# Kernel optimization log

Hardware: AMD Instinct MI355X
Metric: run time of the kernel (lower is better)

The kernel has to match this reference:

```python
import jax, jax.numpy as jnp
import numpy as np

C = 256
GROUPS = 8
EPS = 1e-5

def group_norm(x, gamma, beta):
    # x: [B, C, L]
    B, Cc, L = x.shape
    xg = x.reshape(B, GROUPS, Cc // GROUPS, L)
    mu = xg.mean(axis=(2, 3), keepdims=True)
    var = xg.var(axis=(2, 3), keepdims=True)
    xn = (xg - mu) / jnp.sqrt(var + EPS)
    xn = xn.reshape(B, Cc, L)
    return xn * gamma[None, :, None] + beta[None, :, None]

def conv1x1(x, W, b):
    # W: [Cout, Cin], x: [B, Cin, L]
    return jnp.einsum('oc,bcl->bol', W, x) + b[None, :, None]

def setup_inputs() -> dict:
    key = jax.random.key(0)
    ks = jax.random.split(key, 11)
    s = 1.0 / np.sqrt(C)
    inp = {
        'x': jax.random.normal(ks[0], (8, C, 2048), dtype=jnp.float32),
        'gamma': jnp.ones((C,), jnp.float32),
        'beta': jnp.zeros((C,), jnp.float32),
        'Wq': jax.random.uniform(ks[1], (C, C), jnp.float32, -s, s),
        'bq': jax.random.uniform(ks[2], (C,), jnp.float32, -s, s),
        'Wk': jax.random.uniform(ks[3], (C, C), jnp.float32, -s, s),
        'bk': jax.random.uniform(ks[4], (C,), jnp.float32, -s, s),
        'Wv': jax.random.uniform(ks[5], (C, C), jnp.float32, -s, s),
        'bv': jax.random.uniform(ks[6], (C,), jnp.float32, -s, s),
        'Wo': jax.random.uniform(ks[7], (C, C), jnp.float32, -s, s),
        'bo': jax.random.uniform(ks[8], (C,), jnp.float32, -s, s),
    }
    return inp

def reference(x, gamma, beta, Wq, bq, Wk, bk, Wv, bv, Wo, bo):
    h = group_norm(x, gamma, beta)
    q = conv1x1(h, Wq, bq)  # [B, C, L]
    k = conv1x1(h, Wk, bk)
    v = conv1x1(h, Wv, bv)
    scale = x.shape[1] ** (-0.5)
    attn = jnp.einsum('bci,bcj->bij', q, k) * scale  # [B, L, L]
    attn = jax.nn.softmax(attn, axis=-1)
    out = jnp.einsum('bij,bcj->bci', attn, v)  # [B, C, L]
    out = conv1x1(out, Wo, bo)
    return x + out
```

## Files before the change

### kernel.cpp

```cpp
#include <hip/hip_runtime.h>
#include <hip/hip_bf16.h>
#include <stddef.h>

#define NB 8
#define NC 256
#define NL 2048

typedef __attribute__((ext_vector_type(8))) short s16x8;
typedef __attribute__((ext_vector_type(4))) float f32x4;

__device__ __forceinline__ short f2bs(float x){
  __hip_bfloat16 h = __float2bfloat16(x);
  return __builtin_bit_cast(short, h);
}
__device__ __forceinline__ float bs2f(short x){
  unsigned u = ((unsigned)(unsigned short)x) << 16;
  return __builtin_bit_cast(float, u);
}

#define MFMA16(a,b,c) __builtin_amdgcn_mfma_f32_16x16x32_bf16((a),(b),(c),0,0,0)

__global__ void k_prep(const float* __restrict__ wq, const float* __restrict__ wk,
                       const float* __restrict__ wv, const float* __restrict__ wo,
                       short* __restrict__ wout){
  int idx = blockIdx.x * 256 + threadIdx.x;
  int which = idx >> 16;
  int off = idx & 65535;
  const float* src = (which == 0) ? wq : (which == 1) ? wk : (which == 2) ? wv : wo;
  float sc = (which == 0) ? 0.0625f : 1.0f;
  wout[idx] = f2bs(src[off] * sc);
}

__global__ __launch_bounds__(256) void k_stats(const float* __restrict__ x, float* __restrict__ gpart){
  const int idx = blockIdx.x;
  const float4* base = (const float4*)(x + (size_t)idx * 8192);
  const int t = threadIdx.x;
  float s = 0.f, ss = 0.f;
  for (int i = t; i < 2048; i += 256){
    float4 v = base[i];
    s  += v.x + v.y + v.z + v.w;
    ss += v.x*v.x + v.y*v.y + v.z*v.z + v.w*v.w;
  }
  #pragma unroll
  for (int m = 32; m; m >>= 1){ s += __shfl_down(s, m); ss += __shfl_down(ss, m); }
  __shared__ float red[8];
  if ((t & 63) == 0){ red[t >> 6] = s; red[4 + (t >> 6)] = ss; }
  __syncthreads();
  if (t == 0){
    gpart[idx * 2 + 0] = red[0] + red[1] + red[2] + red[3];
    gpart[idx * 2 + 1] = red[4] + red[5] + red[6] + red[7];
  }
}

__global__ __launch_bounds__(256) void k_gapply(const float* __restrict__ x, const float* __restrict__ gamma,
                                                const float* __restrict__ beta, const float* __restrict__ gpart,
                                                short* __restrict__ ht){
  const int idx = blockIdx.x;
  const int bg = idx >> 3, lt8 = idx & 7;
  const int b = bg >> 3, g = bg & 7;
  float S = 0.f, SS = 0.f;
  #pragma unroll
  for (int s2 = 0; s2 < 8; ++s2){ S += gpart[(bg * 8 + s2) * 2]; SS += gpart[(bg * 8 + s2) * 2 + 1]; }
  const float mu = S * (1.f / 65536.f);
  const float var = SS * (1.f / 65536.f) - mu * mu;
  const float rstd = rsqrtf(var + 1e-5f);
  const float* xg = x + (size_t)bg * 65536;
  const int t = threadIdx.x;
  const int cc = t >> 3, lch = t & 7;
  const int c = g * 32 + cc;
  const float gsc = gamma[c] * rstd;
  const float gbi = beta[c] - mu * gsc;
  __shared__ short tile[64 * 33];
  const int ll_s = t & 63, cg = t >> 6;
  for (int lt = 0; lt < 4; ++lt){
    const int l0 = lt8 * 256 + lt * 64;
    const float4* rp = (const float4*)(xg + (size_t)cc * NL + l0 + lch * 8);
    float4 a = rp[0], bv = rp[1];
    float vals[8] = {a.x, a.y, a.z, a.w, bv.x, bv.y, bv.z, bv.w};
    short o[8];
    #pragma unroll
    for (int e = 0; e < 8; ++e) o[e] = f2bs(vals[e] * gsc + gbi);
    __syncthreads();
    #pragma unroll
    for (int e = 0; e < 8; ++e) tile[(lch * 8 + e) * 33 + cc] = o[e];
    __syncthreads();
    s16x8 pk;
    #pragma unroll
    for (int e = 0; e < 8; ++e) pk[e] = tile[ll_s * 33 + cg * 8 + e];
    *(s16x8*)(ht + ((size_t)(b * NL) + l0 + ll_s) * NC + g * 32 + cg * 8) = pk;
  }
}

__global__ __launch_bounds__(256) void k_conv_qk(const short* __restrict__ ht, const short* __restrict__ wbf,
                                                 const float* __restrict__ bq, const float* __restrict__ bk,
                                                 short* __restrict__ qt, short* __restrict__ kt){
  const int b = blockIdx.z & 7, which = blockIdx.z >> 3;
  const short* wmat = wbf + (which ? 65536 : 0);
  const float* bias = which ? bk : bq;
  const float bsc = which ? 1.0f : 0.0625f;
  short* outp = which ? kt : qt;
  const int lane = threadIdx.x & 63, wid = threadIdx.x >> 6;
  const int wr = wid >> 1, wc = wid & 1;
  const int l0 = blockIdx.y * 128 + wr * 64;
  const int o0 = blockIdx.x * 64 + wc * 32;
  const int kgrp = (lane >> 4) * 8;
  const short* aptr = ht + ((size_t)(b * NL) + l0 + (lane & 15)) * NC + kgrp;
  const short* bptr = wmat + (size_t)(o0 + (lane & 15)) * NC + kgrp;
  f32x4 acc[4][2];
  #pragma unroll
  for (int i = 0; i < 4; ++i){
    #pragma unroll
    for (int j = 0; j < 2; ++j){ f32x4 z = {0.f,0.f,0.f,0.f}; acc[i][j] = z; }
  }
  #pragma unroll 2
  for (int kk = 0; kk < 256; kk += 32){
    s16x8 af[4], bfr[2];
    #pragma unroll
    for (int mf = 0; mf < 4; ++mf) af[mf] = *(const s16x8*)(aptr + (size_t)(mf * 16) * NC + kk);
    #pragma unroll
    for (int nf = 0; nf < 2; ++nf) bfr[nf] = *(const s16x8*)(bptr + (size_t)(nf * 16) * NC + kk);
    #pragma unroll
    for (int mf = 0; mf < 4; ++mf)
      #pragma unroll
      for (int nf = 0; nf < 2; ++nf)
        acc[mf][nf] = MFMA16(af[mf], bfr[nf], acc[mf][nf]);
  }
  #pragma unroll
  for (int nf = 0; nf < 2; ++nf){
    const int oc = o0 + nf * 16 + (lane & 15);
    const float bb = bias[oc] * bsc;
    #pragma unroll
    for (int mf = 0; mf < 4; ++mf){
      #pragma unroll
      for (int r = 0; r < 4; ++r){
        const int lr = l0 + mf * 16 + (lane >> 4) * 4 + r;
        outp[((size_t)(b * NL) + lr) * NC + oc] = f2bs(acc[mf][nf][r] + bb);
      }
    }
  }
}

__global__ __launch_bounds__(256) void k_conv_v(const short* __restrict__ ht, const short* __restrict__ wv,
                                                const float* __restrict__ bv, short* __restrict__ vout){
  const int b = blockIdx.z;
  const int lane = threadIdx.x & 63, wid = threadIdx.x >> 6;
  const int wr = wid >> 1, wc = wid & 1;
  const int o0 = blockIdx.y * 128 + wr * 64;
  const int l0 = blockIdx.x * 64 + wc * 32;
  const int kgrp = (lane >> 4) * 8;
  const short* aptr = wv + (size_t)(o0 + (lane & 15)) * NC + kgrp;
  const short* bptr = ht + ((size_t)(b * NL) + l0 + (lane & 15)) * NC + kgrp;
  f32x4 acc[4][2];
  #pragma unroll
  for (int i = 0; i < 4; ++i){
    #pragma unroll
    for (int j = 0; j < 2; ++j){ f32x4 z = {0.f,0.f,0.f,0.f}; acc[i][j] = z; }
  }
  #pragma unroll 2
  for (int kk = 0; kk < 256; kk += 32){
    s16x8 af[4], bfr[2];
    #pragma unroll
    for (int mf = 0; mf < 4; ++mf) af[mf] = *(const s16x8*)(aptr + (size_t)(mf * 16) * NC + kk);
    #pragma unroll
    for (int nf = 0; nf < 2; ++nf) bfr[nf] = *(const s16x8*)(bptr + (size_t)(nf * 16) * NC + kk);
    #pragma unroll
    for (int mf = 0; mf < 4; ++mf)
      #pragma unroll
      for (int nf = 0; nf < 2; ++nf)
        acc[mf][nf] = MFMA16(af[mf], bfr[nf], acc[mf][nf]);
  }
  #pragma unroll
  for (int mf = 0; mf < 4; ++mf){
    #pragma unroll
    for (int r = 0; r < 4; ++r){
      const int orow = o0 + mf * 16 + (lane >> 4) * 4 + r;
      const float bb = bv[orow];
      #pragma unroll
      for (int nf = 0; nf < 2; ++nf){
        const int lcol = l0 + nf * 16 + (lane & 15);
        vout[((size_t)(b * NC) + orow) * NL + lcol] = f2bs(acc[mf][nf][r] + bb);
      }
    }
  }
}

__global__ __launch_bounds__(256, 2) void k_flash(const short* __restrict__ qt, const short* __restrict__ kt,
                                                  const short* __restrict__ v, short* __restrict__ po,
                                                  float* __restrict__ ml){
  const int flat = blockIdx.x;
  const int b = flat & 7;
  const int rest = flat >> 3;
  const int h = rest & 1;
  const int i0 = (rest >> 1) * 64;
  const int lane = threadIdx.x & 63, wid = threadIdx.x >> 6;
  __shared__ short k_lds[64 * 256];
  __shared__ short v_lds[256 * 64];
  __shared__ short plds[4][1024];
  short* pl = plds[wid];
  const int arow = lane & 15, kg = lane >> 4;

  const short* qp = qt + ((size_t)(b * NL) + i0 + wid * 16 + arow) * NC + kg * 8;
  s16x8 qf[8];
  #pragma unroll
  for (int kc = 0; kc < 8; ++kc) qf[kc] = *(const s16x8*)(qp + kc * 32);

  f32x4 oacc[16];
  #pragma unroll
  for (int i = 0; i < 16; ++i){ f32x4 z = {0.f,0.f,0.f,0.f}; oacc[i] = z; }
  float m_r[4], l_r[4];
  #pragma unroll
  for (int r = 0; r < 4; ++r){ m_r[r] = -3.0e38f; l_r[r] = 0.f; }

  auto STAGE_K = [&](int jt){
    const int j0 = jt * 64;
    #pragma unroll
    for (int t = 0; t < 8; ++t){
      const int i = wid * 8 + t;
      const int r = 2 * i + (lane >> 5);
      const int wb = (lane & 31) * 16;
      const short* src = kt + ((size_t)(b * NL) + j0 + r) * NC + ((wb ^ ((r & 15) << 4)) >> 1);
      __builtin_amdgcn_global_load_lds((const __attribute__((address_space(1))) void*)src,
                                       (__attribute__((address_space(3))) void*)&k_lds[i * 512], 16, 0, 0);
    }
  };
  auto STAGE_V = [&](int jt){
    const int j0 = jt * 64;
    #pragma unroll
    for (int t = 0; t < 8; ++t){
      const int i = wid * 8 + t;
      const int rc = 8 * i + (lane >> 3);
      const int wb = (lane & 7) * 16;
      const short* src = v + ((size_t)(b * NC) + rc) * NL + j0 + ((wb ^ ((rc & 7) << 4)) >> 1);
      __builtin_amdgcn_global_load_lds((const __attribute__((address_space(1))) void*)src,
                                       (__attribute__((address_space(3))) void*)&v_lds[i * 512], 16, 0, 0);
    }
  };

  const int jb0 = h * 16, jend = jb0 + 16;
  STAGE_K(jb0);
  STAGE_V(jb0);
  asm volatile("s_waitcnt vmcnt(0)" ::: "memory");
  __builtin_amdgcn_s_barrier();
  __builtin_amdgcn_sched_barrier(0);

  for (int jt = jb0; jt < jend; ++jt){
    f32x4 sf[4];
    #pragma unroll
    for (int nf = 0; nf < 4; ++nf){ f32x4 z = {0.f,0.f,0.f,0.f}; sf[nf] = z; }
    __builtin_amdgcn_s_setprio(1);
    #pragma unroll
    for (int kc = 0; kc < 8; ++kc){
      #pragma unroll
      for (int nf = 0; nf < 4; ++nf){
        const int r = nf * 16 + arow;
        s16x8 kf = *(const s16x8*)&k_lds[r * 256 + (((kc * 64 + kg * 16) ^ ((arow & 15) << 4)) >> 1)];
        sf[nf] = MFMA16(qf[kc], kf, sf[nf]);
      }
    }
    __builtin_amdgcn_s_setprio(0);
    float corr[4];
    #pragma unroll
    for (int r = 0; r < 4; ++r){
      float mx = fmaxf(fmaxf(sf[0][r], sf[1][r]), fmaxf(sf[2][r], sf[3][r]));
      #pragma unroll
      for (int d = 1; d < 16; d <<= 1) mx = fmaxf(mx, __shfl_xor(mx, d));
      const float mn = fmaxf(m_r[r], mx);
      corr[r] = __expf(m_r[r] - mn);
      float rs = 0.f;
      #pragma unroll
      for (int nf = 0; nf < 4; ++nf){
        float p = __expf(sf[nf][r] - mn);
        sf[nf][r] = p;
        rs += p;
      }
      #pragma unroll
      for (int d = 1; d < 16; d <<= 1) rs += __shfl_xor(rs, d);
      l_r[r] = l_r[r] * corr[r] + rs;
      m_r[r] = mn;
    }
    #pragma unroll
    for (int i = 0; i < 16; ++i){
      f32x4 t = oacc[i];
      t[0] *= corr[0]; t[1] *= corr[1]; t[2] *= corr[2]; t[3] *= corr[3];
      oacc[i] = t;
    }
    asm volatile("s_waitcnt vmcnt(0)" ::: "memory");
    __builtin_amdgcn_s_barrier();
    __builtin_amdgcn_sched_barrier(0);
    if (jt + 1 < jend) STAGE_K(jt + 1);

    #pragma unroll
    for (int r = 0; r < 4; ++r){
      const int rowp = kg * 4 + r;
      const int swz = (rowp & 7) << 3;
      #pragma unroll
      for (int nf = 0; nf < 4; ++nf){
        const int col = nf * 16 + arow;
        pl[rowp * 64 + (col ^ swz)] = f2bs(sf[nf][r]);
      }
    }
    __builtin_amdgcn_s_setprio(1);
    #pragma unroll
    for (int kc2 = 0; kc2 < 2; ++kc2){
      const int swz2 = (arow & 7) << 3;
      s16x8 pa = *(const s16x8*)(pl + arow * 64 + ((kc2 * 32 + kg * 8) ^ swz2));
      #pragma unroll
      for (int nf2 = 0; nf2 < 16; ++nf2){
        const int rc = nf2 * 16 + arow;
        s16x8 vf = *(const s16x8*)&v_lds[rc * 64 + (((kc2 * 64 + kg * 16) ^ ((rc & 7) << 4)) >> 1)];
        oacc[nf2] = MFMA16(pa, vf, oacc[nf2]);
      }
    }
    __builtin_amdgcn_s_setprio(0);
    __builtin_amdgcn_s_barrier();
    __builtin_amdgcn_sched_barrier(0);
    if (jt + 1 < jend) STAGE_V(jt + 1);
    asm volatile("s_waitcnt vmcnt(8)" ::: "memory");
    __builtin_amdgcn_s_barrier();
    __builtin_amdgcn_sched_barrier(0);
  }

  short* pob = po + (size_t)h * 4194304 + ((size_t)(b * NL) + i0 + wid * 16) * NC;
  #pragma unroll
  for (int r = 0; r < 4; ++r){
    const int irow = kg * 4 + r;
    #pragma unroll
    for (int nf2 = 0; nf2 < 16; ++nf2){
      pob[(size_t)irow * NC + nf2 * 16 + arow] = f2bs(oacc[nf2][r]);
    }
    if (arow == 0){
      const size_t Rg = (size_t)h * 16384 + (size_t)(b * NL) + i0 + wid * 16 + irow;
      ml[Rg * 2 + 0] = m_r[r];
      ml[Rg * 2 + 1] = l_r[r];
    }
  }
}

__global__ __launch_bounds__(256) void k_final(const short* __restrict__ po, const float* __restrict__ ml,
                                               const short* __restrict__ wo, const float* __restrict__ bo,
                                               const float* __restrict__ x, float* __restrict__ out){
  const int b = blockIdx.z;
  const int lane = threadIdx.x & 63, wid = threadIdx.x >> 6;
  const int wr = wid >> 1, wc = wid & 1;
  const int o0 = blockIdx.y * 128 + wr * 64;
  const int i0 = blockIdx.x * 64 + wc * 32;
  const int kgrp = (lane >> 4) * 8;
  const short* aptr = wo + (size_t)(o0 + (lane & 15)) * NC + kgrp;
  float wgt[2][2], winv[2];
  size_t rbase[2];
  #pragma unroll
  for (int nf = 0; nf < 2; ++nf){
    const int Rg = b * NL + i0 + nf * 16 + (lane & 15);
    rbase[nf] = (size_t)Rg * NC + kgrp;
    const float m0 = ml[(size_t)Rg * 2],             l0 = ml[(size_t)Rg * 2 + 1];
    const float m1 = ml[((size_t)16384 + Rg) * 2],   l1 = ml[((size_t)16384 + Rg) * 2 + 1];
    const float mm = fmaxf(m0, m1);
    wgt[nf][0] = __expf(m0 - mm);
    wgt[nf][1] = __expf(m1 - mm);
    winv[nf] = 1.f / (l0 * wgt[nf][0] + l1 * wgt[nf][1]);
  }
  f32x4 acc[4][2];
  #pragma unroll
  for (int i = 0; i < 4; ++i){
    #pragma unroll
    for (int j = 0; j < 2; ++j){ f32x4 z = {0.f,0.f,0.f,0.f}; acc[i][j] = z; }
  }
  for (int kk = 0; kk < 256; kk += 32){
    s16x8 af[4], bfr[2];
    #pragma unroll
    for (int mf = 0; mf < 4; ++mf) af[mf] = *(const s16x8*)(aptr + (size_t)(mf * 16) * NC + kk);
    #pragma unroll
    for (int nf = 0; nf < 2; ++nf){
      s16x8 p0 = *(const s16x8*)(po + rbase[nf] + kk);
      s16x8 p1 = *(const s16x8*)(po + (size_t)4194304 + rbase[nf] + kk);
      #pragma unroll
      for (int e = 0; e < 8; ++e)
        bfr[nf][e] = f2bs((wgt[nf][0] * bs2f(p0[e]) + wgt[nf][1] * bs2f(p1[e])) * winv[nf]);
    }
    #pragma unroll
    for (int mf = 0; mf < 4; ++mf)
      #pragma unroll
      for (int nf = 0; nf < 2; ++nf)
        acc[mf][nf] = MFMA16(af[mf], bfr[nf], acc[mf][nf]);
  }
  #pragma unroll
  for (int mf = 0; mf < 4; ++mf){
    #pragma unroll
    for (int r = 0; r < 4; ++r){
      const int orow = o0 + mf * 16 + (lane >> 4) * 4 + r;
      const float bb = bo[orow];
      #pragma unroll
      for (int nf = 0; nf < 2; ++nf){
        const int icol = i0 + nf * 16 + (lane & 15);
        const size_t idx = ((size_t)(b * NC) + orow) * NL + icol;
        out[idx] = acc[mf][nf][r] + bb + x[idx];
      }
    }
  }
}

extern "C" void kernel_launch(void* const* d_in, const int* in_sizes, int n_in,
                              void* d_out, int out_size, void* d_ws, size_t ws_size,
                              hipStream_t stream){
  const float* x     = (const float*)d_in[0];
  const float* gamma = (const float*)d_in[1];
  const float* beta  = (const float*)d_in[2];
  const float* Wq    = (const float*)d_in[3];
  const float* bq    = (const float*)d_in[4];
  const float* Wk    = (const float*)d_in[5];
  const float* bk    = (const float*)d_in[6];
  const float* Wv    = (const float*)d_in[7];
  const float* bv    = (const float*)d_in[8];
  const float* Wo    = (const float*)d_in[9];
  const float* bo    = (const float*)d_in[10];
  float* out = (float*)d_out;

  char* ws = (char*)d_ws;
  short* wbf = (short*)ws;
  short* ht  = (short*)(ws + (size_t)524288);
  short* qt  = (short*)(ws + (size_t)524288 + 8388608);
  short* ktp = (short*)(ws + (size_t)524288 + 2 * 8388608);
  short* vp  = (short*)(ws + (size_t)524288 + 3 * 8388608);
  short* pop = (short*)(ws + (size_t)524288 + 4 * 8388608);
  float* mlp = (float*)(ws + (size_t)524288 + 6 * 8388608);
  float* gpp = (float*)(ws + (size_t)524288 + 6 * 8388608 + 262144);

  k_prep  <<<1024, 256, 0, stream>>>(Wq, Wk, Wv, Wo, wbf);
  k_stats <<<512, 256, 0, stream>>>(x, gpp);
  k_gapply<<<512, 256, 0, stream>>>(x, gamma, beta, gpp, ht);
  k_conv_qk<<<dim3(4, 16, 16), 256, 0, stream>>>(ht, wbf, bq, bk, qt, ktp);
  k_conv_v <<<dim3(32, 2, 8), 256, 0, stream>>>(ht, wbf + 2 * 65536, bv, vp);
  k_flash  <<<dim3(512), 256, 0, stream>>>(qt, ktp, vp, pop, mlp);
  k_final  <<<dim3(32, 2, 8), 256, 0, stream>>>(pop, mlp, wbf + 3 * 65536, bo, x, out);
}
```

Baseline: 142.2 us.

## Merge weight prep into stats, fuse QKV convs, add lazy softmax rescaling

Folds the weight-conversion kernel into the group-stats kernel as extra blocks, and merges the separate Q/K and V projection kernels into one launch using the z index to pick the layout. This removes two kernel launches and their tail gaps. In the flash kernel, the running-max update and accumulator rescale are skipped when no row's new max exceeds the stored max by more than 8. That saves exp calls and 64 multiplies per tile, but stale maxima can let exponentials grow to about e^8 before the final normalization.

```diff
diff --git a/kernel.cpp b/kernel.cpp
--- a/kernel.cpp
+++ b/kernel.cpp
@@ -20,21 +20,22 @@
 
 #define MFMA16(a,b,c) __builtin_amdgcn_mfma_f32_16x16x32_bf16((a),(b),(c),0,0,0)
 
-__global__ void k_prep(const float* __restrict__ wq, const float* __restrict__ wk,
-                       const float* __restrict__ wv, const float* __restrict__ wo,
-                       short* __restrict__ wout){
-  int idx = blockIdx.x * 256 + threadIdx.x;
-  int which = idx >> 16;
-  int off = idx & 65535;
-  const float* src = (which == 0) ? wq : (which == 1) ? wk : (which == 2) ? wv : wo;
-  float sc = (which == 0) ? 0.0625f : 1.0f;
-  wout[idx] = f2bs(src[off] * sc);
-}
-
-__global__ __launch_bounds__(256) void k_stats(const float* __restrict__ x, float* __restrict__ gpart){
+__global__ __launch_bounds__(256) void k_stats_prep(const float* __restrict__ x, float* __restrict__ gpart,
+                                                    const float* __restrict__ wq, const float* __restrict__ wk,
+                                                    const float* __restrict__ wv, const float* __restrict__ wo,
+                                                    short* __restrict__ wout){
+  const int t = threadIdx.x;
+  if (blockIdx.x >= 512){
+    int idx = (blockIdx.x - 512) * 256 + t;
+    int which = idx >> 16;
+    int off = idx & 65535;
+    const float* src = (which == 0) ? wq : (which == 1) ? wk : (which == 2) ? wv : wo;
+    float sc = (which == 0) ? 0.0625f : 1.0f;
+    wout[idx] = f2bs(src[off] * sc);
+    return;
+  }
   const int idx = blockIdx.x;
   const float4* base = (const float4*)(x + (size_t)idx * 8192);
-  const int t = threadIdx.x;
   float s = 0.f, ss = 0.f;
   for (int i = t; i < 2048; i += 256){
     float4 v = base[i];
@@ -91,26 +92,36 @@
   }
 }
 
-__global__ __launch_bounds__(256) void k_conv_qk(const short* __restrict__ ht, const short* __restrict__ wbf,
-                                                 const float* __restrict__ bq, const float* __restrict__ bk,
-                                                 short* __restrict__ qt, short* __restrict__ kt){
-  const int b = blockIdx.z & 7, which = blockIdx.z >> 3;
-  const short* wmat = wbf + (which ? 65536 : 0);
-  const float* bias = which ? bk : bq;
-  const float bsc = which ? 1.0f : 0.0625f;
-  short* outp = which ? kt : qt;
+__global__ __launch_bounds__(256) void k_conv_qkv(const short* __restrict__ ht, const short* __restrict__ wbf,
+                                                  const float* __restrict__ bq, const float* __restrict__ bk,
+                                                  const float* __restrict__ bv,
+                                                  short* __restrict__ qt, short* __restrict__ kt,
+                                                  short* __restrict__ vt){
+  const int z = blockIdx.z;
+  const int b = z & 7, which = z >> 3;
   const int lane = threadIdx.x & 63, wid = threadIdx.x >> 6;
   const int wr = wid >> 1, wc = wid & 1;
-  const int l0 = blockIdx.y * 128 + wr * 64;
-  const int o0 = blockIdx.x * 64 + wc * 32;
   const int kgrp = (lane >> 4) * 8;
-  const short* aptr = ht + ((size_t)(b * NL) + l0 + (lane & 15)) * NC + kgrp;
-  const short* bptr = wmat + (size_t)(o0 + (lane & 15)) * NC + kgrp;
+  const short* aptr;
+  const short* bptr;
+  int m0, n0;
+  if (which < 2){
+    m0 = blockIdx.y * 128 + wr * 64;
+    n0 = blockIdx.x * 64 + wc * 32;
+    aptr = ht + ((size_t)(b * NL) + m0 + (lane & 15)) * NC + kgrp;
+    bptr = wbf + (which ? 65536 : 0) + (size_t)(n0 + (lane & 15)) * NC + kgrp;
+  } else {
+    const int idx = blockIdx.y * 4 + blockIdx.x;
+    m0 = (idx >> 5) * 128 + wr * 64;
+    n0 = (idx & 31) * 64 + wc * 32;
+    aptr = wbf + 2 * 65536 + (size_t)(m0 + (lane & 15)) * NC + kgrp;
+    bptr = ht + ((size_t)(b * NL) + n0 + (lane & 15)) * NC + kgrp;
+  }
   f32x4 acc[4][2];
   #pragma unroll
   for (int i = 0; i < 4; ++i){
     #pragma unroll
-    for (int j = 0; j < 2; ++j){ f32x4 z = {0.f,0.f,0.f,0.f}; acc[i][j] = z; }
+    for (int j = 0; j < 2; ++j){ f32x4 z2 = {0.f,0.f,0.f,0.f}; acc[i][j] = z2; }
   }
   #pragma unroll 2
   for (int kk = 0; kk < 256; kk += 32){
@@ -125,60 +136,35 @@
       for (int nf = 0; nf < 2; ++nf)
         acc[mf][nf] = MFMA16(af[mf], bfr[nf], acc[mf][nf]);
   }
-  #pragma unroll
-  for (int nf = 0; nf < 2; ++nf){
-    const int oc = o0 + nf * 16 + (lane & 15);
-    const float bb = bias[oc] * bsc;
+  if (which < 2){
+    const float* bias = which ? bk : bq;
+    const float bsc = which ? 1.0f : 0.0625f;
+    short* outp = which ? kt : qt;
+    #pragma unroll
+    for (int nf = 0; nf < 2; ++nf){
+      const int oc = n0 + nf * 16 + (lane & 15);
+      const float bb = bias[oc] * bsc;
+      #pragma unroll
+      for (int mf = 0; mf < 4; ++mf){
+        #pragma unroll
+        for (int r = 0; r < 4; ++r){
+          const int lr = m0 + mf * 16 + (lane >> 4) * 4 + r;
+          outp[((size_t)(b * NL) + lr) * NC + oc] = f2bs(acc[mf][nf][r] + bb);
+        }
+      }
+    }
+  } else {
     #pragma unroll
     for (int mf = 0; mf < 4; ++mf){
       #pragma unroll
       for (int r = 0; r < 4; ++r){
-        const int lr = l0 + mf * 16 + (lane >> 4) * 4 + r;
-        outp[((size_t)(b * NL) + lr) * NC + oc] = f2bs(acc[mf][nf][r] + bb);
-      }
-    }
-  }
-}
-
-__global__ __launch_bounds__(256) void k_conv_v(const short* __restrict__ ht, const short* __restrict__ wv,
-                                                const float* __restrict__ bv, short* __restrict__ vout){
-  const int b = blockIdx.z;
-  const int lane = threadIdx.x & 63, wid = threadIdx.x >> 6;
-  const int wr = wid >> 1, wc = wid & 1;
-  const int o0 = blockIdx.y * 128 + wr * 64;
-  const int l0 = blockIdx.x * 64 + wc * 32;
-  const int kgrp = (lane >> 4) * 8;
-  const short* aptr = wv + (size_t)(o0 + (lane & 15)) * NC + kgrp;
-  const short* bptr = ht + ((size_t)(b * NL) + l0 + (lane & 15)) * NC + kgrp;
-  f32x4 acc[4][2];
-  #pragma unroll
-  for (int i = 0; i < 4; ++i){
-    #pragma unroll
-    for (int j = 0; j < 2; ++j){ f32x4 z = {0.f,0.f,0.f,0.f}; acc[i][j] = z; }
-  }
-  #pragma unroll 2
-  for (int kk = 0; kk < 256; kk += 32){
-    s16x8 af[4], bfr[2];
-    #pragma unroll
-    for (int mf = 0; mf < 4; ++mf) af[mf] = *(const s16x8*)(aptr + (size_t)(mf * 16) * NC + kk);
-    #pragma unroll
-    for (int nf = 0; nf < 2; ++nf) bfr[nf] = *(const s16x8*)(bptr + (size_t)(nf * 16) * NC + kk);
-    #pragma unroll
-    for (int mf = 0; mf < 4; ++mf)
-      #pragma unroll
-      for (int nf = 0; nf < 2; ++nf)
-        acc[mf][nf] = MFMA16(af[mf], bfr[nf], acc[mf][nf]);
-  }
-  #pragma unroll
-  for (int mf = 0; mf < 4; ++mf){
-    #pragma unroll
-    for (int r = 0; r < 4; ++r){
-      const int orow = o0 + mf * 16 + (lane >> 4) * 4 + r;
-      const float bb = bv[orow];
-      #pragma unroll
-      for (int nf = 0; nf < 2; ++nf){
-        const int lcol = l0 + nf * 16 + (lane & 15);
-        vout[((size_t)(b * NC) + orow) * NL + lcol] = f2bs(acc[mf][nf][r] + bb);
+        const int orow = m0 + mf * 16 + (lane >> 4) * 4 + r;
+        const float bb = bv[orow];
+        #pragma unroll
+        for (int nf = 0; nf < 2; ++nf){
+          const int lcol = n0 + nf * 16 + (lane & 15);
+          vt[((size_t)(b * NC) + orow) * NL + lcol] = f2bs(acc[mf][nf][r] + bb);
+        }
       }
     }
   }
@@ -258,31 +244,44 @@
       }
     }
     __builtin_amdgcn_s_setprio(0);
-    float corr[4];
+    float mx[4];
     #pragma unroll
     for (int r = 0; r < 4; ++r){
-      float mx = fmaxf(fmaxf(sf[0][r], sf[1][r]), fmaxf(sf[2][r], sf[3][r]));
-      #pragma unroll
-      for (int d = 1; d < 16; d <<= 1) mx = fmaxf(mx, __shfl_xor(mx, d));
-      const float mn = fmaxf(m_r[r], mx);
-      corr[r] = __expf(m_r[r] - mn);
+      float m2 = fmaxf(fmaxf(sf[0][r], sf[1][r]), fmaxf(sf[2][r], sf[3][r]));
+      #pragma unroll
+      for (int d = 1; d < 16; d <<= 1) m2 = fmaxf(m2, __shfl_xor(m2, d));
+      mx[r] = m2;
+    }
+    const int ok = (mx[0] <= m_r[0] + 8.f) & (mx[1] <= m_r[1] + 8.f) &
+                   (mx[2] <= m_r[2] + 8.f) & (mx[3] <= m_r[3] + 8.f);
+    if (!__all(ok)){
+      float corr[4];
+      #pragma unroll
+      for (int r = 0; r < 4; ++r){
+        const float mn = fmaxf(m_r[r], mx[r]);
+        corr[r] = __expf(m_r[r] - mn);
+        m_r[r] = mn;
+        l_r[r] *= corr[r];
+      }
+      #pragma unroll
+      for (int i = 0; i < 16; ++i){
+        f32x4 t = oacc[i];
+        t[0] *= corr[0]; t[1] *= corr[1]; t[2] *= corr[2]; t[3] *= corr[3];
+        oacc[i] = t;
+      }
+    }
+    #pragma unroll
+    for (int r = 0; r < 4; ++r){
       float rs = 0.f;
       #pragma unroll
       for (int nf = 0; nf < 4; ++nf){
-        float p = __expf(sf[nf][r] - mn);
+        float p = __expf(sf[nf][r] - m_r[r]);
         sf[nf][r] = p;
         rs += p;
       }
       #pragma unroll
       for (int d = 1; d < 16; d <<= 1) rs += __shfl_xor(rs, d);
-      l_r[r] = l_r[r] * corr[r] + rs;
-      m_r[r] = mn;
-    }
-    #pragma unroll
-    for (int i = 0; i < 16; ++i){
-      f32x4 t = oacc[i];
-      t[0] *= corr[0]; t[1] *= corr[1]; t[2] *= corr[2]; t[3] *= corr[3];
-      oacc[i] = t;
+      l_r[r] += rs;
     }
     asm volatile("s_waitcnt vmcnt(0)" ::: "memory");
     __builtin_amdgcn_s_barrier();
@@ -425,11 +424,9 @@
   float* mlp = (float*)(ws + (size_t)524288 + 6 * 8388608);
   float* gpp = (float*)(ws + (size_t)524288 + 6 * 8388608 + 262144);
 
-  k_prep  <<<1024, 256, 0, stream>>>(Wq, Wk, Wv, Wo, wbf);
-  k_stats <<<512, 256, 0, stream>>>(x, gpp);
+  k_stats_prep<<<1536, 256, 0, stream>>>(x, gpp, Wq, Wk, Wv, Wo, wbf);
   k_gapply<<<512, 256, 0, stream>>>(x, gamma, beta, gpp, ht);
-  k_conv_qk<<<dim3(4, 16, 16), 256, 0, stream>>>(ht, wbf, bq, bk, qt, ktp);
-  k_conv_v <<<dim3(32, 2, 8), 256, 0, stream>>>(ht, wbf + 2 * 65536, bv, vp);
+  k_conv_qkv<<<dim3(4, 16, 24), 256, 0, stream>>>(ht, wbf, bq, bk, bv, qt, ktp, vp);
   k_flash  <<<dim3(512), 256, 0, stream>>>(qt, ktp, vp, pop, mlp);
   k_final  <<<dim3(32, 2, 8), 256, 0, stream>>>(pop, mlp, wbf + 3 * 65536, bo, x, out);
 }
```

Measured after the change: 133.1 us. -6.4%, faster.
